# Kernel tuning notes

Hardware: AMD Instinct MI355X
Metric: run time of the kernel (lower is better)

## Reference

```python
import jax, jax.numpy as jnp
import numpy as np

B, S, D, DK = 4, 2048, 1024, 1024


def setup_inputs() -> dict:
    key = jax.random.key(0)
    kx, kq, kk, kv = jax.random.split(key, 4)
    return {
        "x": jax.random.normal(kx, (B, S, D), dtype=jnp.float32),
        "WQ": jax.random.normal(kq, (D, DK), dtype=jnp.float32),
        "WK": jax.random.normal(kk, (D, DK), dtype=jnp.float32),
        "WV": jax.random.normal(kv, (D, DK), dtype=jnp.float32),
    }


def reference(x, WQ, WK, WV):
    # q,k,v: [B,S,DK]
    q = x @ WQ
    k = x @ WK
    v = x @ WV
    scale = 1.0 / np.sqrt(DK).astype(np.float32)
    scores = jnp.einsum("bqd,bkd->bqk", q, k) * scale  # [B,S,S]
    # NOTE: original uses nn.Softmax(dim=1) -> normalize over the QUERY axis (axis 1)
    attn = jax.nn.softmax(scores, axis=1)
    return jnp.einsum("bqk,bkd->bqd", attn, v)
```

## Files before the change

kernel.cpp:

```cpp
#include <hip/hip_runtime.h>

constexpr int Bc  = 4;
constexpr int Sc  = 2048;
constexpr int Dc  = 1024;
constexpr int DKc = 1024;
constexpr long BSc = (long)Bc * Sc;

typedef __attribute__((ext_vector_type(8))) __bf16 bf16x8;
typedef __attribute__((ext_vector_type(4))) float  floatx4;

__device__ inline __bf16 f2bf(float f) {
  unsigned u = __builtin_bit_cast(unsigned, f);
  u = (u + 0x7FFFu + ((u >> 16) & 1u)) >> 16;
  unsigned short s = (unsigned short)u;
  return __builtin_bit_cast(__bf16, s);
}
__device__ inline float bf2f(__bf16 h) {
  unsigned u = ((unsigned)__builtin_bit_cast(unsigned short, h)) << 16;
  return __builtin_bit_cast(float, u);
}

__device__ inline void stage16(const __bf16* g, __bf16* l) {
  __builtin_amdgcn_global_load_lds(
      (const __attribute__((address_space(1))) unsigned int*)g,
      (__attribute__((address_space(3))) unsigned int*)l, 16, 0, 0);
}

__device__ __forceinline__ void bar_raw() {
  asm volatile("" ::: "memory");
  __builtin_amdgcn_s_barrier();
  asm volatile("" ::: "memory");
}
template <int N>
__device__ __forceinline__ void vmwait() {
  asm volatile("s_waitcnt vmcnt(%0)" :: "n"(N));
  __builtin_amdgcn_sched_barrier(0);
}

__global__ __launch_bounds__(256) void prep(
    const float* __restrict__ x,  __bf16* __restrict__ xhi, __bf16* __restrict__ xlo,
    const float* __restrict__ wq, __bf16* __restrict__ qhi, __bf16* __restrict__ qlo,
    const float* __restrict__ wk, __bf16* __restrict__ khi, __bf16* __restrict__ klo,
    const float* __restrict__ wv, __bf16* __restrict__ vthi) {
  __shared__ float tile[32][33];
  long blk = blockIdx.x;
  if (blk >= 40960) {
    int t   = (int)(blk - 40960);
    int bx  = t & 31, by = t >> 5;
    int thx = threadIdx.x & 31, thy = threadIdx.x >> 5;
    int xI  = bx * 32 + thx, yI = by * 32 + thy;
#pragma unroll
    for (int j = 0; j < 32; j += 8)
      tile[thy + j][thx] = wv[(long)(yI + j) * DKc + xI];
    __syncthreads();
    int xO = by * 32 + thx, yO = bx * 32 + thy;
#pragma unroll
    for (int j = 0; j < 32; j += 8)
      vthi[(long)(yO + j) * Dc + xO] = f2bf(tile[thx][thy + j]);
    return;
  }
  const float* in; __bf16 *hi, *lo; long base;
  if (blk < 32768)      { in = x;  hi = xhi; lo = xlo; base = blk * 256; }
  else if (blk < 36864) { in = wq; hi = qhi; lo = qlo; base = (blk - 32768) * 256; }
  else                  { in = wk; hi = khi; lo = klo; base = (blk - 36864) * 256; }
  long i = base + threadIdx.x;
  float f = in[i];
  __bf16 h = f2bf(f);
  hi[i] = h;
  lo[i] = f2bf(f - bf2f(h));
}

enum { MODE_V = 1 };
constexpr int VSTR = 136;

template <int MODE>
__device__ __forceinline__ void gemm_body(
    char* smem,
    const __bf16* __restrict__ Ahi,
    const __bf16* __restrict__ Bhi,
    __bf16* __restrict__ Chi) {
  constexpr int  K = Dc;
  __bf16* sAh = (__bf16*)smem;
  __bf16* sBh = sAh + 128 * 32;

  const int wave = threadIdx.x >> 6;
  const int lane = threadIdx.x & 63;
  const int wm   = wave >> 1;
  const int wn   = wave & 1;
  const int m0   = blockIdx.y * 128;
  const int n0   = blockIdx.x * 128;

  const __bf16* Ab  = Ahi + (long)m0 * K;
  const __bf16* Bb  = Bhi + (long)n0 * K;

  const int sr   = lane >> 2;
  const int sc_  = lane & 3;
  const int scol = (sc_ ^ ((sr >> 1) & 3)) * 8;

  floatx4 acc[4][4];
  const floatx4 zero = {0.f, 0.f, 0.f, 0.f};
#pragma unroll
  for (int i = 0; i < 4; ++i)
#pragma unroll
    for (int j = 0; j < 4; ++j) acc[i][j] = zero;

  const int frow = lane & 15;
  const int pko = ((lane >> 4) ^ ((frow >> 1) & 3)) * 8;

#pragma unroll 1
  for (int k0 = 0; k0 < K; k0 += 32) {
#pragma unroll
    for (int i = 0; i < 2; ++i) {
      const int rb = wave * 32 + i * 16;
      const long go = (long)(rb + sr) * K + k0 + scol;
      stage16(Ab + go, sAh + rb * 32);
      stage16(Bb + go, sBh + rb * 32);
    }
    __syncthreads();

    bf16x8 af[4], bfr[4];
#pragma unroll
    for (int t = 0; t < 4; ++t) {
      af[t]  = *(const bf16x8*)(sAh + (wm * 64 + t * 16 + frow) * 32 + pko);
      bfr[t] = *(const bf16x8*)(sBh + (wn * 64 + t * 16 + frow) * 32 + pko);
    }
#pragma unroll
    for (int mt = 0; mt < 4; ++mt)
#pragma unroll
      for (int nt = 0; nt < 4; ++nt)
        acc[mt][nt] = __builtin_amdgcn_mfma_f32_16x16x32_bf16(af[mt], bfr[nt], acc[mt][nt], 0, 0, 0);
    __syncthreads();
  }

  const int crow0 = (lane >> 4) * 4;
  const int ccol  = lane & 15;
  const int tid   = threadIdx.x;

  __bf16* sT = (__bf16*)smem;
#pragma unroll
  for (int nt = 0; nt < 4; ++nt) {
    int nl = wn * 64 + nt * 16 + ccol;
#pragma unroll
    for (int mt = 0; mt < 4; ++mt) {
      int ml = wm * 64 + mt * 16 + crow0;
#pragma unroll
      for (int r = 0; r < 4; ++r)
        sT[(long)nl * VSTR + ml + r] = f2bf(acc[mt][nt][r]);
    }
  }
  __syncthreads();
  const int bb   = m0 >> 11;
  const int seq0 = m0 & (Sc - 1);
  __bf16* dst = Chi + (long)bb * DKc * Sc + seq0;
#pragma unroll
  for (int c = 0; c < 8; ++c) {
    int flat = c * 2048 + tid * 8;
    int row = flat >> 7, col = flat & 127;
    *(bf16x8*)(dst + (long)(n0 + row) * Sc + col) =
        *(const bf16x8*)(sT + (long)row * VSTR + col);
  }
}

__global__ __launch_bounds__(256) void gemm_v(
    const __bf16* __restrict__ xhi, const __bf16* __restrict__ wvthi,
    __bf16* __restrict__ vt) {
  __shared__ __align__(16) char smem[128 * VSTR * 2];
  gemm_body<MODE_V>(smem, xhi, wvthi, vt);
}

struct SCtx {
  const __bf16 *pAh, *pAl, *pBh, *pBl;
  __bf16* lds;
  int stLds;
  int aoff, boff;
};

template <int WA, int WB, int WC, bool SAL, bool S2A, bool S2B>
__device__ __forceinline__ void tile_step(const SCtx& c, int t,
                                          floatx4 (&acc)[8][4]) {
  constexpr int K = 1024;
  constexpr int BH = 8192, BL = 16384, AL = 24576;
  __bf16* cur = c.lds + (t & 1) * 32768;
  __bf16* oth = c.lds + ((t & 1) ^ 1) * 32768;
  bf16x8 af[8], bfr[4];

  vmwait<WA>();
  bar_raw();
#pragma unroll
  for (int mt = 0; mt < 8; ++mt)
    af[mt] = *(const bf16x8*)(cur + c.aoff + mt * 512);
#pragma unroll
  for (int nt = 0; nt < 4; ++nt)
    bfr[nt] = *(const bf16x8*)(cur + BH + c.boff + nt * 512);
  if (SAL) {
    const __bf16* s = c.pAl + (t + 1) * 32;
    stage16(s, oth + AL + c.stLds);
    stage16(s + 16 * K, oth + AL + c.stLds + 512);
  }
  bar_raw();
  __builtin_amdgcn_s_setprio(1);
#pragma unroll
  for (int mt = 0; mt < 8; ++mt)
#pragma unroll
    for (int nt = 0; nt < 4; ++nt)
      acc[mt][nt] = __builtin_amdgcn_mfma_f32_16x16x32_bf16(af[mt], bfr[nt], acc[mt][nt], 0, 0, 0);
  __builtin_amdgcn_s_setprio(0);

  vmwait<WB>();
  bar_raw();
  {
    bf16x8 bfl[4];
#pragma unroll
    for (int nt = 0; nt < 4; ++nt)
      bfl[nt] = *(const bf16x8*)(cur + BL + c.boff + nt * 512);
    if (S2A) {
      const __bf16* sa = c.pAh + (t + 2) * 32;
      stage16(sa, cur + c.stLds);
      stage16(sa + 16 * K, cur + c.stLds + 512);
      stage16(c.pBh + (t + 2) * 32, cur + BH + c.stLds);
    }
    bar_raw();
    __builtin_amdgcn_s_setprio(1);
#pragma unroll
    for (int mt = 0; mt < 8; ++mt)
#pragma unroll
      for (int nt = 0; nt < 4; ++nt)
        acc[mt][nt] = __builtin_amdgcn_mfma_f32_16x16x32_bf16(af[mt], bfl[nt], acc[mt][nt], 0, 0, 0);
    __builtin_amdgcn_s_setprio(0);
  }

  vmwait<WC>();
  bar_raw();
  {
    bf16x8 afl[8];
#pragma unroll
    for (int mt = 0; mt < 8; ++mt)
      afl[mt] = *(const bf16x8*)(cur + AL + c.aoff + mt * 512);
    if (S2B) {
      stage16(c.pBh + (t + 2) * 32 + 16 * K, cur + BH + c.stLds + 512);
      const __bf16* sb = c.pBl + (t + 2) * 32;
      stage16(sb, cur + BL + c.stLds);
      stage16(sb + 16 * K, cur + BL + c.stLds + 512);
    }
    bar_raw();
    __builtin_amdgcn_s_setprio(1);
#pragma unroll
    for (int mt = 0; mt < 8; ++mt)
#pragma unroll
      for (int nt = 0; nt < 4; ++nt)
        acc[mt][nt] = __builtin_amdgcn_mfma_f32_16x16x32_bf16(afl[mt], bfr[nt], acc[mt][nt], 0, 0, 0);
    __builtin_amdgcn_s_setprio(0);
  }
}

__global__ __launch_bounds__(512, 2) void gemm_s2(
    const __bf16* __restrict__ thi, const __bf16* __restrict__ tlo,
    const __bf16* __restrict__ xhi, const __bf16* __restrict__ xlo,
    __bf16* __restrict__ P, float* __restrict__ Pmax, float* __restrict__ Psum) {
  __shared__ __align__(16) __bf16 smem[65536];
  constexpr int K = 1024;
  const int b    = blockIdx.z;
  const int m0   = blockIdx.y * 256;
  const int n0   = blockIdx.x * 256;
  const int wave = threadIdx.x >> 6;
  const int lane = threadIdx.x & 63;
  const int wm   = wave >> 2;
  const int wn   = wave & 3;
  const int sr   = lane >> 2;
  const int scol = ((lane & 3) ^ ((sr >> 1) & 3)) * 8;
  const int frow = lane & 15;
  const int pko  = ((lane >> 4) ^ ((frow >> 1) & 3)) * 8;

  SCtx c;
  const long batch = (long)Sc * 1024;
  const long ar = (long)(m0 + wave * 32 + sr) * K + scol;
  const long br = (long)(n0 + wave * 32 + sr) * K + scol;
  c.pAh = thi + (long)b * batch + ar;
  c.pAl = tlo + (long)b * batch + ar;
  c.pBh = xhi + (long)b * batch + br;
  c.pBl = xlo + (long)b * batch + br;
  c.lds = smem;
  c.stLds = wave * 1024;
  c.aoff = (wm * 128 + frow) * 32 + pko;
  c.boff = (wn * 64 + frow) * 32 + pko;

  {
    __bf16* b0 = smem;
    __bf16* b1 = smem + 32768;
    stage16(c.pAh, b0 + c.stLds);               stage16(c.pAh + 16 * K, b0 + c.stLds + 512);
    stage16(c.pBh, b0 + 8192 + c.stLds);        stage16(c.pBh + 16 * K, b0 + 8192 + c.stLds + 512);
    stage16(c.pBl, b0 + 16384 + c.stLds);       stage16(c.pBl + 16 * K, b0 + 16384 + c.stLds + 512);
    stage16(c.pAl, b0 + 24576 + c.stLds);       stage16(c.pAl + 16 * K, b0 + 24576 + c.stLds + 512);
    stage16(c.pAh + 32, b1 + c.stLds);          stage16(c.pAh + 32 + 16 * K, b1 + c.stLds + 512);
    stage16(c.pBh + 32, b1 + 8192 + c.stLds);   stage16(c.pBh + 32 + 16 * K, b1 + 8192 + c.stLds + 512);
    stage16(c.pBl + 32, b1 + 16384 + c.stLds);  stage16(c.pBl + 32 + 16 * K, b1 + 16384 + c.stLds + 512);
  }

  floatx4 acc[8][4];
  const floatx4 zero = {0.f, 0.f, 0.f, 0.f};
#pragma unroll
  for (int i = 0; i < 8; ++i)
#pragma unroll
    for (int j = 0; j < 4; ++j) acc[i][j] = zero;

#pragma unroll 1
  for (int t = 0; t < 30; ++t) tile_step<10, 10, 11, true, true, true>(c, t, acc);
  tile_step<10, 10, 8, true, false, false>(c, 30, acc);
  tile_step<4, 2, 0, false, false, false>(c, 31, acc);

  const int crow0 = (lane >> 4) * 4;
  const int ccol  = lane & 15;
  const int tid   = threadIdx.x;
  constexpr float scale = 0.03125f;
  float* smax = (float*)smem;
  float* ssum = smax + 512;

  float cm[4];
#pragma unroll
  for (int nt = 0; nt < 4; ++nt) {
    float mx = -3.0e38f;
#pragma unroll
    for (int mt = 0; mt < 8; ++mt)
#pragma unroll
      for (int r = 0; r < 4; ++r) mx = fmaxf(mx, acc[mt][nt][r] * scale);
    cm[nt] = mx;
  }
#pragma unroll
  for (int off = 16; off <= 32; off <<= 1)
#pragma unroll
    for (int nt = 0; nt < 4; ++nt)
      cm[nt] = fmaxf(cm[nt], __shfl_xor(cm[nt], off, 64));
  __syncthreads();
  if (lane < 16)
#pragma unroll
    for (int nt = 0; nt < 4; ++nt)
      smax[wm * 256 + wn * 64 + nt * 16 + lane] = cm[nt];
  __syncthreads();
  float mfin[4];
#pragma unroll
  for (int nt = 0; nt < 4; ++nt) {
    int cidx = wn * 64 + nt * 16 + ccol;
    mfin[nt] = fmaxf(smax[cidx], smax[256 + cidx]);
  }
  float ps[4];
#pragma unroll
  for (int nt = 0; nt < 4; ++nt) {
    float s = 0.f;
#pragma unroll
    for (int mt = 0; mt < 8; ++mt)
#pragma unroll
      for (int r = 0; r < 4; ++r)
        s += __expf(acc[mt][nt][r] * scale - mfin[nt]);
    ps[nt] = s;
  }
#pragma unroll
  for (int off = 16; off <= 32; off <<= 1)
#pragma unroll
    for (int nt = 0; nt < 4; ++nt) ps[nt] += __shfl_xor(ps[nt], off, 64);
  if (lane < 16)
#pragma unroll
    for (int nt = 0; nt < 4; ++nt)
      ssum[wm * 256 + wn * 64 + nt * 16 + lane] = ps[nt];
  __syncthreads();
  if (tid < 256) {
    long o = ((long)b * 8 + blockIdx.y) * Sc + n0 + tid;
    Pmax[o] = fmaxf(smax[tid], smax[256 + tid]);
    Psum[o] = ssum[tid] + ssum[256 + tid];
  }
  __syncthreads();
  __bf16* sT = smem;
#pragma unroll
  for (int nt = 0; nt < 4; ++nt) {
    int col = wn * 64 + nt * 16 + ccol;
#pragma unroll
    for (int mt = 0; mt < 8; ++mt) {
      int rowb = wm * 128 + mt * 16 + crow0;
#pragma unroll
      for (int r = 0; r < 4; ++r) {
        int row = rowb + r;
        sT[row * 256 + (col ^ (((row >> 2) & 3) << 4))] =
            f2bf(__expf(acc[mt][nt][r] * scale - mfin[nt]));
      }
    }
  }
  __syncthreads();
  __bf16* Pb = P + (long)b * ((long)Sc * Sc);
#pragma unroll
  for (int cc = 0; cc < 16; ++cc) {
    int flat = cc * 4096 + tid * 8;
    int row = flat >> 8, col = flat & 255;
    *(bf16x8*)(Pb + (long)(m0 + row) * Sc + n0 + col) =
        *(const bf16x8*)(sT + row * 256 + (col ^ (((row >> 2) & 3) << 4)));
  }
}

struct TCtx {
  const __bf16 *pAh, *pAl, *pBh, *pBl;
  __bf16* lds;
  int stA, stB;
  int aoff, boff;
};

template <int WA, int WB, int WC, bool SAL, bool S2AB, bool S2B>
__device__ __forceinline__ void tile_step_t(const TCtx& c, int t,
                                            floatx4 (&acc)[4][4]) {
  constexpr int K = 1024;
  constexpr int BH = 8192, BL = 12288, AL = 16384, BUF = 24576;
  __bf16* cur = c.lds + (t & 1) * BUF;
  __bf16* oth = c.lds + ((t & 1) ^ 1) * BUF;
  bf16x8 af[4], bfr[4];

  vmwait<WA>();
  bar_raw();
#pragma unroll
  for (int mt = 0; mt < 4; ++mt)
    af[mt] = *(const bf16x8*)(cur + c.aoff + mt * 512);
#pragma unroll
  for (int nt = 0; nt < 4; ++nt)
    bfr[nt] = *(const bf16x8*)(cur + BH + c.boff + nt * 512);
  if (SAL) {
    const __bf16* s = c.pAl + (t + 1) * 32;
    stage16(s, oth + AL + c.stA);
    stage16(s + 16 * K, oth + AL + c.stA + 512);
  }
  bar_raw();
  __builtin_amdgcn_s_setprio(1);
#pragma unroll
  for (int mt = 0; mt < 4; ++mt)
#pragma unroll
    for (int nt = 0; nt < 4; ++nt)
      acc[mt][nt] = __builtin_amdgcn_mfma_f32_16x16x32_bf16(af[mt], bfr[nt], acc[mt][nt], 0, 0, 0);
  __builtin_amdgcn_s_setprio(0);

  vmwait<WB>();
  bar_raw();
  {
    bf16x8 bfl[4];
#pragma unroll
    for (int nt = 0; nt < 4; ++nt)
      bfl[nt] = *(const bf16x8*)(cur + BL + c.boff + nt * 512);
    if (S2AB) {
      const __bf16* sa = c.pAh + (t + 2) * 32;
      stage16(sa, cur + c.stA);
      stage16(sa + 16 * K, cur + c.stA + 512);
      stage16(c.pBh + (t + 2) * 32, cur + BH + c.stB);
    }
    bar_raw();
    __builtin_amdgcn_s_setprio(1);
#pragma unroll
    for (int mt = 0; mt < 4; ++mt)
#pragma unroll
      for (int nt = 0; nt < 4; ++nt)
        acc[mt][nt] = __builtin_amdgcn_mfma_f32_16x16x32_bf16(af[mt], bfl[nt], acc[mt][nt], 0, 0, 0);
    __builtin_amdgcn_s_setprio(0);
  }

  vmwait<WC>();
  bar_raw();
  {
    bf16x8 afl[4];
#pragma unroll
    for (int mt = 0; mt < 4; ++mt)
      afl[mt] = *(const bf16x8*)(cur + AL + c.aoff + mt * 512);
    if (S2B) stage16(c.pBl + (t + 2) * 32, cur + BL + c.stB);
    bar_raw();
    __builtin_amdgcn_s_setprio(1);
#pragma unroll
    for (int mt = 0; mt < 4; ++mt)
#pragma unroll
      for (int nt = 0; nt < 4; ++nt)
        acc[mt][nt] = __builtin_amdgcn_mfma_f32_16x16x32_bf16(afl[mt], bfr[nt], acc[mt][nt], 0, 0, 0);
    __builtin_amdgcn_s_setprio(0);
  }
}

__global__ __launch_bounds__(512, 2) void gemm_t2(
    const __bf16* __restrict__ xhi, const __bf16* __restrict__ xlo,
    const __bf16* __restrict__ gthi, const __bf16* __restrict__ gtlo,
    __bf16* __restrict__ thi, __bf16* __restrict__ tlo) {
  __shared__ __align__(16) __bf16 smem[49152];
  constexpr int K = 1024;
  const int m0   = blockIdx.y * 256;
  const int n0   = blockIdx.x * 128;
  const int wave = threadIdx.x >> 6;
  const int lane = threadIdx.x & 63;
  const int wm   = wave >> 1;
  const int wn   = wave & 1;
  const int sr   = lane >> 2;
  const int scol = ((lane & 3) ^ ((sr >> 1) & 3)) * 8;
  const int frow = lane & 15;
  const int pko  = ((lane >> 4) ^ ((frow >> 1) & 3)) * 8;

  TCtx c;
  const long ar = (long)(m0 + wave * 32 + sr) * K + scol;
  const long br = (long)(n0 + wave * 16 + sr) * K + scol;
  c.pAh = xhi + ar;
  c.pAl = xlo + ar;
  c.pBh = gthi + br;
  c.pBl = gtlo + br;
  c.lds = smem;
  c.stA = wave * 1024;
  c.stB = wave * 512;
  c.aoff = (wm * 64 + frow) * 32 + pko;
  c.boff = (wn * 64 + frow) * 32 + pko;

  {
    __bf16* b0 = smem;
    __bf16* b1 = smem + 24576;
    stage16(c.pAh, b0 + c.stA);          stage16(c.pAh + 16 * K, b0 + c.stA + 512);
    stage16(c.pBh, b0 + 8192 + c.stB);
    stage16(c.pBl, b0 + 12288 + c.stB);
    stage16(c.pAl, b0 + 16384 + c.stA);  stage16(c.pAl + 16 * K, b0 + 16384 + c.stA + 512);
    stage16(c.pAh + 32, b1 + c.stA);     stage16(c.pAh + 32 + 16 * K, b1 + c.stA + 512);
    stage16(c.pBh + 32, b1 + 8192 + c.stB);
    stage16(c.pBl + 32, b1 + 12288 + c.stB);
  }

  floatx4 acc[4][4];
  const floatx4 zero = {0.f, 0.f, 0.f, 0.f};
#pragma unroll
  for (int i = 0; i < 4; ++i)
#pragma unroll
    for (int j = 0; j < 4; ++j) acc[i][j] = zero;

#pragma unroll 1
  for (int t = 0; t < 30; ++t) tile_step_t<7, 8, 9, true, true, true>(c, t, acc);
  tile_step_t<7, 8, 6, true, false, false>(c, 30, acc);
  tile_step_t<3, 2, 0, false, false, false>(c, 31, acc);

  const int crow0 = (lane >> 4) * 4;
  const int ccol  = lane & 15;
  const int tid   = threadIdx.x;
  __bf16* sT = smem;
#pragma unroll 1
  for (int pass = 0; pass < 2; ++pass) {
    __syncthreads();
#pragma unroll
    for (int nt = 0; nt < 4; ++nt) {
      int col = wn * 64 + nt * 16 + ccol;
#pragma unroll
      for (int mt = 0; mt < 4; ++mt) {
        int rowb = wm * 64 + mt * 16 + crow0;
#pragma unroll
        for (int r = 0; r < 4; ++r) {
          int row = rowb + r;
          float v = acc[mt][nt][r];
          __bf16 h = f2bf(v);
          sT[row * 128 + (col ^ (((row >> 2) & 3) << 4))] =
              pass ? f2bf(v - bf2f(h)) : h;
        }
      }
    }
    __syncthreads();
    __bf16* dst = pass ? tlo : thi;
#pragma unroll
    for (int cc = 0; cc < 8; ++cc) {
      int flat = cc * 4096 + tid * 8;
      int row = flat >> 7, col = flat & 127;
      *(bf16x8*)(dst + (long)(m0 + row) * DKc + n0 + col) =
          *(const bf16x8*)(sT + row * 128 + (col ^ (((row >> 2) & 3) << 4)));
    }
  }
}

__global__ __launch_bounds__(256) void scale_p(__bf16* __restrict__ P,
                                               const float* __restrict__ ffac) {
  long i8 = (long)blockIdx.x * 256 + threadIdx.x;
  long base = i8 * 8;
  int k = (int)(base & (Sc - 1));
  int q = (int)((base >> 11) & (Sc - 1));
  int b = (int)(base >> 22);
  int t = q >> 8;
  const float* f = ffac + (((long)b * 8 + t) << 11) + k;
  float4 f0 = *(const float4*)f;
  float4 f1 = *(const float4*)(f + 4);
  bf16x8 p = *(const bf16x8*)(P + base);
  bf16x8 o;
  o[0] = f2bf(bf2f(p[0]) * f0.x);
  o[1] = f2bf(bf2f(p[1]) * f0.y);
  o[2] = f2bf(bf2f(p[2]) * f0.z);
  o[3] = f2bf(bf2f(p[3]) * f0.w);
  o[4] = f2bf(bf2f(p[4]) * f1.x);
  o[5] = f2bf(bf2f(p[5]) * f1.y);
  o[6] = f2bf(bf2f(p[6]) * f1.z);
  o[7] = f2bf(bf2f(p[7]) * f1.w);
  *(bf16x8*)(P + base) = o;
}

struct PCtx {
  const __bf16 *pA, *pB;
  int stA, stB;
  int aoff, boff;
};

template <int WA, int WB, bool STG>
__device__ __forceinline__ void tile_step_pv(const PCtx& c, int t,
                                             __bf16* cur, __bf16* dst,
                                             floatx4 (&acc)[4][4]) {
  constexpr int K = 2048;
  vmwait<WA>();
  bar_raw();
  {
    bf16x8 af[4], bfr[4];
#pragma unroll
    for (int mt = 0; mt < 4; ++mt)
      af[mt] = *(const bf16x8*)(cur + c.aoff + mt * 512);
#pragma unroll
    for (int nt = 0; nt < 4; ++nt)
      bfr[nt] = *(const bf16x8*)(cur + 16384 + c.boff + nt * 512);
    if (STG) {
      const __bf16* a = c.pA + (t + 2) * 64;
      stage16(a, dst + c.stA);
      stage16(a + 16 * K, dst + c.stA + 512);
      stage16(c.pB + (t + 2) * 64, dst + 16384 + c.stB);
    }
    bar_raw();
    __builtin_amdgcn_s_setprio(1);
#pragma unroll
    for (int mt = 0; mt < 4; ++mt)
#pragma unroll
      for (int nt = 0; nt < 4; ++nt)
        acc[mt][nt] = __builtin_amdgcn_mfma_f32_16x16x32_bf16(af[mt], bfr[nt], acc[mt][nt], 0, 0, 0);
    __builtin_amdgcn_s_setprio(0);
  }
  vmwait<WB>();
  bar_raw();
  {
    bf16x8 af[4], bfr[4];
#pragma unroll
    for (int mt = 0; mt < 4; ++mt)
      af[mt] = *(const bf16x8*)(cur + 8192 + c.aoff + mt * 512);
#pragma unroll
    for (int nt = 0; nt < 4; ++nt)
      bfr[nt] = *(const bf16x8*)(cur + 20480 + c.boff + nt * 512);
    if (STG) {
      const __bf16* a = c.pA + (t + 2) * 64 + 32;
      stage16(a, dst + 8192 + c.stA);
      stage16(a + 16 * K, dst + 8192 + c.stA + 512);
      stage16(c.pB + (t + 2) * 64 + 32, dst + 20480 + c.stB);
    }
    bar_raw();
    __builtin_amdgcn_s_setprio(1);
#pragma unroll
    for (int mt = 0; mt < 4; ++mt)
#pragma unroll
      for (int nt = 0; nt < 4; ++nt)
        acc[mt][nt] = __builtin_amdgcn_mfma_f32_16x16x32_bf16(af[mt], bfr[nt], acc[mt][nt], 0, 0, 0);
    __builtin_amdgcn_s_setprio(0);
  }
}

__global__ __launch_bounds__(512, 2) void gemm_pv2(
    const __bf16* __restrict__ P, const __bf16* __restrict__ vt,
    float* __restrict__ out) {
  __shared__ __align__(16) __bf16 smem[73728];
  constexpr int K = 2048;
  const int b    = blockIdx.z;
  const int m0   = blockIdx.x * 256;
  const int n0   = blockIdx.y * 128;
  const int wave = threadIdx.x >> 6;
  const int lane = threadIdx.x & 63;
  const int wm   = wave >> 1;
  const int wn   = wave & 1;
  const int sr   = lane >> 2;
  const int scol = ((lane & 3) ^ ((sr >> 1) & 3)) * 8;
  const int frow = lane & 15;
  const int pko  = ((lane >> 4) ^ ((frow >> 1) & 3)) * 8;

  PCtx c;
  c.pA = P + (long)b * Sc * Sc + (long)(m0 + wave * 32 + sr) * K + scol;
  c.pB = vt + (long)b * DKc * Sc + (long)(n0 + wave * 16 + sr) * K + scol;
  c.stA = wave * 1024;
  c.stB = wave * 512;
  c.aoff = (wm * 64 + frow) * 32 + pko;
  c.boff = (wn * 64 + frow) * 32 + pko;

  __bf16* B0 = smem;
  __bf16* B1 = smem + 24576;
  __bf16* B2 = smem + 49152;

  stage16(c.pA, B0 + c.stA);            stage16(c.pA + 16 * K, B0 + c.stA + 512);
  stage16(c.pB, B0 + 16384 + c.stB);
  stage16(c.pA + 32, B0 + 8192 + c.stA); stage16(c.pA + 32 + 16 * K, B0 + 8192 + c.stA + 512);
  stage16(c.pB + 32, B0 + 20480 + c.stB);
  stage16(c.pA + 64, B1 + c.stA);       stage16(c.pA + 64 + 16 * K, B1 + c.stA + 512);
  stage16(c.pB + 64, B1 + 16384 + c.stB);
  stage16(c.pA + 96, B1 + 8192 + c.stA); stage16(c.pA + 96 + 16 * K, B1 + 8192 + c.stA + 512);
  stage16(c.pB + 96, B1 + 20480 + c.stB);

  floatx4 acc[4][4];
  const floatx4 zero = {0.f, 0.f, 0.f, 0.f};
#pragma unroll
  for (int i = 0; i < 4; ++i)
#pragma unroll
    for (int j = 0; j < 4; ++j) acc[i][j] = zero;

#pragma unroll 1
  for (int t = 0; t < 30; t += 3) {
    tile_step_pv<9, 9, true>(c, t,     B0, B2, acc);
    tile_step_pv<9, 9, true>(c, t + 1, B1, B0, acc);
    tile_step_pv<9, 9, true>(c, t + 2, B2, B1, acc);
  }
  tile_step_pv<9, 6, false>(c, 30, B0, B0, acc);
  tile_step_pv<3, 0, false>(c, 31, B1, B1, acc);

  const int crow0 = (lane >> 4) * 4;
  const int ccol  = lane & 15;
#pragma unroll
  for (int nt = 0; nt < 4; ++nt) {
    int cn = n0 + wn * 64 + nt * 16 + ccol;
#pragma unroll
    for (int mt = 0; mt < 4; ++mt) {
#pragma unroll
      for (int r = 0; r < 4; ++r) {
        int cm_ = m0 + wm * 64 + mt * 16 + crow0 + r;
        out[(long)b * Sc * DKc + (long)cm_ * DKc + cn] = acc[mt][nt][r];
      }
    }
  }
}

__global__ __launch_bounds__(256) void gemm_g64(
    const __bf16* __restrict__ Ahi, const __bf16* __restrict__ Alo,
    const __bf16* __restrict__ Bhi, const __bf16* __restrict__ Blo,
    __bf16* __restrict__ Chi, __bf16* __restrict__ Clo) {
  constexpr int K = Dc, N = DKc;
  __shared__ __align__(16) char smem[16384];
  __bf16* sAh = (__bf16*)smem;
  __bf16* sBh = sAh + 64 * 32;
  __bf16* sAl = sBh + 64 * 32;
  __bf16* sBl = sAl + 64 * 32;

  const int wave = threadIdx.x >> 6;
  const int lane = threadIdx.x & 63;
  const int wm   = wave >> 1, wn = wave & 1;
  const int m0   = blockIdx.y * 64;
  const int n0   = blockIdx.x * 64;

  const int sr   = lane >> 2;
  const int sc_  = lane & 3;
  const int scol = (sc_ ^ ((sr >> 1) & 3)) * 8;
  const int frow = lane & 15;
  const int pko  = ((lane >> 4) ^ ((frow >> 1) & 3)) * 8;

  floatx4 acc[2][2];
  const floatx4 zero = {0.f, 0.f, 0.f, 0.f};
#pragma unroll
  for (int i = 0; i < 2; ++i)
#pragma unroll
    for (int j = 0; j < 2; ++j) acc[i][j] = zero;

#pragma unroll 1
  for (int k0 = 0; k0 < K; k0 += 32) {
    const int rb = wave * 16;
    const long ga = (long)(m0 + rb + sr) * K + k0 + scol;
    const long gb = (long)(n0 + rb + sr) * K + k0 + scol;
    stage16(Ahi + ga, sAh + rb * 32);
    stage16(Alo + ga, sAl + rb * 32);
    stage16(Bhi + gb, sBh + rb * 32);
    stage16(Blo + gb, sBl + rb * 32);
    __syncthreads();

    bf16x8 af[2], bfr[2], afl[2], bfl[2];
#pragma unroll
    for (int t = 0; t < 2; ++t) {
      af[t]  = *(const bf16x8*)(sAh + (wm * 32 + t * 16 + frow) * 32 + pko);
      bfr[t] = *(const bf16x8*)(sBh + (wn * 32 + t * 16 + frow) * 32 + pko);
      afl[t] = *(const bf16x8*)(sAl + (wm * 32 + t * 16 + frow) * 32 + pko);
      bfl[t] = *(const bf16x8*)(sBl + (wn * 32 + t * 16 + frow) * 32 + pko);
    }
#pragma unroll
    for (int mt = 0; mt < 2; ++mt)
#pragma unroll
      for (int nt = 0; nt < 2; ++nt) {
        acc[mt][nt] = __builtin_amdgcn_mfma_f32_16x16x32_bf16(af[mt], bfr[nt], acc[mt][nt], 0, 0, 0);
        acc[mt][nt] = __builtin_amdgcn_mfma_f32_16x16x32_bf16(af[mt], bfl[nt], acc[mt][nt], 0, 0, 0);
        acc[mt][nt] = __builtin_amdgcn_mfma_f32_16x16x32_bf16(afl[mt], bfr[nt], acc[mt][nt], 0, 0, 0);
      }
    __syncthreads();
  }

  const int crow0 = (lane >> 4) * 4;
  const int ccol  = lane & 15;
  const int tid   = threadIdx.x;
  __bf16* sT = (__bf16*)smem;
#pragma unroll 1
  for (int pass = 0; pass < 2; ++pass) {
    __syncthreads();
#pragma unroll
    for (int nt = 0; nt < 2; ++nt) {
      int col = wn * 32 + nt * 16 + ccol;
#pragma unroll
      for (int mt = 0; mt < 2; ++mt) {
        int row = wm * 32 + mt * 16 + crow0;
#pragma unroll
        for (int r = 0; r < 4; ++r) {
          float v = acc[mt][nt][r];
          __bf16 h = f2bf(v);
          sT[(row + r) * 64 + col] = pass ? f2bf(v - bf2f(h)) : h;
        }
      }
    }
    __syncthreads();
    __bf16* dst = pass ? Clo : Chi;
#pragma unroll
    for (int c = 0; c < 2; ++c) {
      int flat = c * 2048 + tid * 8;
      int row = flat >> 6, col = flat & 63;
      *(bf16x8*)(dst + (long)(m0 + row) * N + n0 + col) = *(const bf16x8*)(sT + flat);
    }
  }
}

__global__ __launch_bounds__(256) void softmax_reduce(const float* __restrict__ Pmax,
                                                      const float* __restrict__ Psum,
                                                      float* __restrict__ Ffac) {
  int idx = blockIdx.x * 256 + threadIdx.x;
  int b = idx >> 11, k = idx & (Sc - 1);
  const float* pm = Pmax + (long)b * 8 * Sc + k;
  const float* ps = Psum + (long)b * 8 * Sc + k;
  float M = -3.0e38f;
#pragma unroll
  for (int t = 0; t < 8; ++t) M = fmaxf(M, pm[(long)t * Sc]);
  float S = 0.f;
#pragma unroll
  for (int t = 0; t < 8; ++t)
    S += ps[(long)t * Sc] * __expf(pm[(long)t * Sc] - M);
  float inv = 1.0f / S;
  float* fo = Ffac + (long)b * 8 * Sc + k;
#pragma unroll
  for (int t = 0; t < 8; ++t)
    fo[(long)t * Sc] = __expf(pm[(long)t * Sc] - M) * inv;
}

extern "C" void kernel_launch(void* const* d_in, const int* in_sizes, int n_in,
                              void* d_out, int out_size, void* d_ws, size_t ws_size,
                              hipStream_t stream) {
  const float* x  = (const float*)d_in[0];
  const float* WQ = (const float*)d_in[1];
  const float* WK = (const float*)d_in[2];
  const float* WV = (const float*)d_in[3];
  float* out = (float*)d_out;
  char* ws = (char*)d_ws;
  const long MB = 1024L * 1024L;

  __bf16* xhi  = (__bf16*)(ws + 0 * MB);
  __bf16* xlo  = (__bf16*)(ws + 16 * MB);
  __bf16* wqhi = (__bf16*)(ws + 32 * MB);
  __bf16* wqlo = (__bf16*)(ws + 34 * MB);
  __bf16* wkhi = (__bf16*)(ws + 36 * MB);
  __bf16* wklo = (__bf16*)(ws + 38 * MB);
  __bf16* wvthi= (__bf16*)(ws + 40 * MB);
  __bf16* gthi = (__bf16*)(ws + 44 * MB);
  __bf16* gtlo = (__bf16*)(ws + 46 * MB);
  __bf16* thi  = (__bf16*)(ws + 48 * MB);
  __bf16* tlo  = (__bf16*)(ws + 64 * MB);
  __bf16* vt   = (__bf16*)(ws + 80 * MB);
  __bf16* P    = (__bf16*)(ws + 96 * MB);
  float*  pmax = (float*)(ws + 128 * MB);
  float*  psum = (float*)(ws + 129 * MB);
  float*  ffac = (float*)(ws + 130 * MB);

  prep<<<41984, 256, 0, stream>>>(x, xhi, xlo, WQ, wqhi, wqlo, WK, wkhi, wklo,
                                  WV, wvthi);

  gemm_g64<<<dim3(16, 16), 256, 0, stream>>>(wkhi, wklo, wqhi, wqlo, gthi, gtlo);

  gemm_t2<<<dim3(DKc / 128, BSc / 256, 1), 512, 0, stream>>>(
      xhi, xlo, gthi, gtlo, thi, tlo);

  gemm_v<<<dim3(DKc / 128, BSc / 128, 1), 256, 0, stream>>>(xhi, wvthi, vt);

  gemm_s2<<<dim3(Sc / 256, Sc / 256, Bc), 512, 0, stream>>>(
      thi, tlo, xhi, xlo, P, pmax, psum);

  softmax_reduce<<<32, 256, 0, stream>>>(pmax, psum, ffac);

  scale_p<<<8192, 256, 0, stream>>>(P, ffac);

  gemm_pv2<<<dim3(Sc / 256, DKc / 128, Bc), 512, 0, stream>>>(P, vt, out);
}
```

Before: 341.5 us.

## Pipeline V projection GEMM with triple-buffered async staging and vectorize prep

Measured after the change: 327.2 us. -4.2%, faster.

```diff
diff --git a/kernel.cpp b/kernel.cpp
--- a/kernel.cpp
+++ b/kernel.cpp
@@ -7,6 +7,7 @@
 constexpr long BSc = (long)Bc * Sc;
 
 typedef __attribute__((ext_vector_type(8))) __bf16 bf16x8;
+typedef __attribute__((ext_vector_type(4))) __bf16 bf16x4;
 typedef __attribute__((ext_vector_type(4))) float  floatx4;
 
 __device__ inline __bf16 f2bf(float f) {
@@ -44,8 +45,8 @@
     const float* __restrict__ wv, __bf16* __restrict__ vthi) {
   __shared__ float tile[32][33];
   long blk = blockIdx.x;
-  if (blk >= 40960) {
-    int t   = (int)(blk - 40960);
+  if (blk >= 10240) {
+    int t   = (int)(blk - 10240);
     int bx  = t & 31, by = t >> 5;
     int thx = threadIdx.x & 31, thy = threadIdx.x >> 5;
     int xI  = bx * 32 + thx, yI = by * 32 + thy;
@@ -60,112 +61,17 @@
     return;
   }
   const float* in; __bf16 *hi, *lo; long base;
-  if (blk < 32768)      { in = x;  hi = xhi; lo = xlo; base = blk * 256; }
-  else if (blk < 36864) { in = wq; hi = qhi; lo = qlo; base = (blk - 32768) * 256; }
-  else                  { in = wk; hi = khi; lo = klo; base = (blk - 36864) * 256; }
-  long i = base + threadIdx.x;
-  float f = in[i];
-  __bf16 h = f2bf(f);
-  hi[i] = h;
-  lo[i] = f2bf(f - bf2f(h));
-}
-
-enum { MODE_V = 1 };
-constexpr int VSTR = 136;
-
-template <int MODE>
-__device__ __forceinline__ void gemm_body(
-    char* smem,
-    const __bf16* __restrict__ Ahi,
-    const __bf16* __restrict__ Bhi,
-    __bf16* __restrict__ Chi) {
-  constexpr int  K = Dc;
-  __bf16* sAh = (__bf16*)smem;
-  __bf16* sBh = sAh + 128 * 32;
-
-  const int wave = threadIdx.x >> 6;
-  const int lane = threadIdx.x & 63;
-  const int wm   = wave >> 1;
-  const int wn   = wave & 1;
-  const int m0   = blockIdx.y * 128;
-  const int n0   = blockIdx.x * 128;
-
-  const __bf16* Ab  = Ahi + (long)m0 * K;
-  const __bf16* Bb  = Bhi + (long)n0 * K;
-
-  const int sr   = lane >> 2;
-  const int sc_  = lane & 3;
-  const int scol = (sc_ ^ ((sr >> 1) & 3)) * 8;
-
-  floatx4 acc[4][4];
-  const floatx4 zero = {0.f, 0.f, 0.f, 0.f};
-#pragma unroll
-  for (int i = 0; i < 4; ++i)
-#pragma unroll
-    for (int j = 0; j < 4; ++j) acc[i][j] = zero;
-
-  const int frow = lane & 15;
-  const int pko = ((lane >> 4) ^ ((frow >> 1) & 3)) * 8;
-
-#pragma unroll 1
-  for (int k0 = 0; k0 < K; k0 += 32) {
-#pragma unroll
-    for (int i = 0; i < 2; ++i) {
-      const int rb = wave * 32 + i * 16;
-      const long go = (long)(rb + sr) * K + k0 + scol;
-      stage16(Ab + go, sAh + rb * 32);
-      stage16(Bb + go, sBh + rb * 32);
-    }
-    __syncthreads();
-
-    bf16x8 af[4], bfr[4];
-#pragma unroll
-    for (int t = 0; t < 4; ++t) {
-      af[t]  = *(const bf16x8*)(sAh + (wm * 64 + t * 16 + frow) * 32 + pko);
-      bfr[t] = *(const bf16x8*)(sBh + (wn * 64 + t * 16 + frow) * 32 + pko);
-    }
-#pragma unroll
-    for (int mt = 0; mt < 4; ++mt)
-#pragma unroll
-      for (int nt = 0; nt < 4; ++nt)
-        acc[mt][nt] = __builtin_amdgcn_mfma_f32_16x16x32_bf16(af[mt], bfr[nt], acc[mt][nt], 0, 0, 0);
-    __syncthreads();
-  }
-
-  const int crow0 = (lane >> 4) * 4;
-  const int ccol  = lane & 15;
-  const int tid   = threadIdx.x;
-
-  __bf16* sT = (__bf16*)smem;
-#pragma unroll
-  for (int nt = 0; nt < 4; ++nt) {
-    int nl = wn * 64 + nt * 16 + ccol;
-#pragma unroll
-    for (int mt = 0; mt < 4; ++mt) {
-      int ml = wm * 64 + mt * 16 + crow0;
-#pragma unroll
-      for (int r = 0; r < 4; ++r)
-        sT[(long)nl * VSTR + ml + r] = f2bf(acc[mt][nt][r]);
-    }
-  }
-  __syncthreads();
-  const int bb   = m0 >> 11;
-  const int seq0 = m0 & (Sc - 1);
-  __bf16* dst = Chi + (long)bb * DKc * Sc + seq0;
-#pragma unroll
-  for (int c = 0; c < 8; ++c) {
-    int flat = c * 2048 + tid * 8;
-    int row = flat >> 7, col = flat & 127;
-    *(bf16x8*)(dst + (long)(n0 + row) * Sc + col) =
-        *(const bf16x8*)(sT + (long)row * VSTR + col);
-  }
-}
-
-__global__ __launch_bounds__(256) void gemm_v(
-    const __bf16* __restrict__ xhi, const __bf16* __restrict__ wvthi,
-    __bf16* __restrict__ vt) {
-  __shared__ __align__(16) char smem[128 * VSTR * 2];
-  gemm_body<MODE_V>(smem, xhi, wvthi, vt);
+  if (blk < 8192)      { in = x;  hi = xhi; lo = xlo; base = blk * 1024; }
+  else if (blk < 9216) { in = wq; hi = qhi; lo = qlo; base = (blk - 8192) * 1024; }
+  else                 { in = wk; hi = khi; lo = klo; base = (blk - 9216) * 1024; }
+  long i = base + (long)threadIdx.x * 4;
+  float4 f = *(const float4*)(in + i);
+  __bf16 h0 = f2bf(f.x), h1 = f2bf(f.y), h2 = f2bf(f.z), h3 = f2bf(f.w);
+  bf16x4 hv = {h0, h1, h2, h3};
+  bf16x4 lv = {f2bf(f.x - bf2f(h0)), f2bf(f.y - bf2f(h1)),
+               f2bf(f.z - bf2f(h2)), f2bf(f.w - bf2f(h3))};
+  *(bf16x4*)(hi + i) = hv;
+  *(bf16x4*)(lo + i) = lv;
 }
 
 struct SCtx {
@@ -560,6 +466,68 @@
       *(bf16x8*)(dst + (long)(m0 + row) * DKc + n0 + col) =
           *(const bf16x8*)(sT + row * 128 + (col ^ (((row >> 2) & 3) << 4)));
     }
+  }
+}
+
+struct PCtx {
+  const __bf16 *pA, *pB;
+  int stA, stB;
+  int aoff, boff;
+};
+
+template <int KK, int WA, int WB, bool STG>
+__device__ __forceinline__ void tile_step_pv(const PCtx& c, int t,
+                                             __bf16* cur, __bf16* dst,
+                                             floatx4 (&acc)[4][4]) {
+  vmwait<WA>();
+  bar_raw();
+  {
+    bf16x8 af[4], bfr[4];
+#pragma unroll
+    for (int mt = 0; mt < 4; ++mt)
+      af[mt] = *(const bf16x8*)(cur + c.aoff + mt * 512);
+#pragma unroll
+    for (int nt = 0; nt < 4; ++nt)
+      bfr[nt] = *(const bf16x8*)(cur + 16384 + c.boff + nt * 512);
+    if (STG) {
+      const __bf16* a = c.pA + (t + 2) * 64;
+      stage16(a, dst + c.stA);
+      stage16(a + 16 * KK, dst + c.stA + 512);
+      stage16(c.pB + (t + 2) * 64, dst + 16384 + c.stB);
+    }
+    bar_raw();
+    __builtin_amdgcn_s_setprio(1);
+#pragma unroll
+    for (int mt = 0; mt < 4; ++mt)
+#pragma unroll
+      for (int nt = 0; nt < 4; ++nt)
+        acc[mt][nt] = __builtin_amdgcn_mfma_f32_16x16x32_bf16(af[mt], bfr[nt], acc[mt][nt], 0, 0, 0);
+    __builtin_amdgcn_s_setprio(0);
+  }
+  vmwait<WB>();
+  bar_raw();
+  {
+    bf16x8 af[4], bfr[4];
+#pragma unroll
+    for (int mt = 0; mt < 4; ++mt)
+      af[mt] = *(const bf16x8*)(cur + 8192 + c.aoff + mt * 512);
+#pragma unroll
+    for (int nt = 0; nt < 4; ++nt)
+      bfr[nt] = *(const bf16x8*)(cur + 20480 + c.boff + nt * 512);
+    if (STG) {
+      const __bf16* a = c.pA + (t + 2) * 64 + 32;
+      stage16(a, dst + 8192 + c.stA);
+      stage16(a + 16 * KK, dst + 8192 + c.stA + 512);
+      stage16(c.pB + (t + 2) * 64 + 32, dst + 20480 + c.stB);
+    }
+    bar_raw();
+    __builtin_amdgcn_s_setprio(1);
+#pragma unroll
+    for (int mt = 0; mt < 4; ++mt)
+#pragma unroll
+      for (int nt = 0; nt < 4; ++nt)
+        acc[mt][nt] = __builtin_amdgcn_mfma_f32_16x16x32_bf16(af[mt], bfr[nt], acc[mt][nt], 0, 0, 0);
+    __builtin_amdgcn_s_setprio(0);
   }
 }
 
@@ -587,69 +555,6 @@
   *(bf16x8*)(P + base) = o;
 }
 
-struct PCtx {
-  const __bf16 *pA, *pB;
-  int stA, stB;
-  int aoff, boff;
-};
-
-template <int WA, int WB, bool STG>
-__device__ __forceinline__ void tile_step_pv(const PCtx& c, int t,
-                                             __bf16* cur, __bf16* dst,
-                                             floatx4 (&acc)[4][4]) {
-  constexpr int K = 2048;
-  vmwait<WA>();
-  bar_raw();
-  {
-    bf16x8 af[4], bfr[4];
-#pragma unroll
-    for (int mt = 0; mt < 4; ++mt)
-      af[mt] = *(const bf16x8*)(cur + c.aoff + mt * 512);
-#pragma unroll
-    for (int nt = 0; nt < 4; ++nt)
-      bfr[nt] = *(const bf16x8*)(cur + 16384 + c.boff + nt * 512);
-    if (STG) {
-      const __bf16* a = c.pA + (t + 2) * 64;
-      stage16(a, dst + c.stA);
-      stage16(a + 16 * K, dst + c.stA + 512);
-      stage16(c.pB + (t + 2) * 64, dst + 16384 + c.stB);
-    }
-    bar_raw();
-    __builtin_amdgcn_s_setprio(1);
-#pragma unroll
-    for (int mt = 0; mt < 4; ++mt)
-#pragma unroll
-      for (int nt = 0; nt < 4; ++nt)
-        acc[mt][nt] = __builtin_amdgcn_mfma_f32_16x16x32_bf16(af[mt], bfr[nt], acc[mt][nt], 0, 0, 0);
-    __builtin_amdgcn_s_setprio(0);
-  }
-  vmwait<WB>();
-  bar_raw();
-  {
-    bf16x8 af[4], bfr[4];
-#pragma unroll
-    for (int mt = 0; mt < 4; ++mt)
-      af[mt] = *(const bf16x8*)(cur + 8192 + c.aoff + mt * 512);
-#pragma unroll
-    for (int nt = 0; nt < 4; ++nt)
-      bfr[nt] = *(const bf16x8*)(cur + 20480 + c.boff + nt * 512);
-    if (STG) {
-      const __bf16* a = c.pA + (t + 2) * 64 + 32;
-      stage16(a, dst + 8192 + c.stA);
-      stage16(a + 16 * K, dst + 8192 + c.stA + 512);
-      stage16(c.pB + (t + 2) * 64 + 32, dst + 20480 + c.stB);
-    }
-    bar_raw();
-    __builtin_amdgcn_s_setprio(1);
-#pragma unroll
-    for (int mt = 0; mt < 4; ++mt)
-#pragma unroll
-      for (int nt = 0; nt < 4; ++nt)
-        acc[mt][nt] = __builtin_amdgcn_mfma_f32_16x16x32_bf16(af[mt], bfr[nt], acc[mt][nt], 0, 0, 0);
-    __builtin_amdgcn_s_setprio(0);
-  }
-}
-
 __global__ __launch_bounds__(512, 2) void gemm_pv2(
     const __bf16* __restrict__ P, const __bf16* __restrict__ vt,
     float* __restrict__ out) {
@@ -697,12 +602,12 @@
 
 #pragma unroll 1
   for (int t = 0; t < 30; t += 3) {
-    tile_step_pv<9, 9, true>(c, t,     B0, B2, acc);
-    tile_step_pv<9, 9, true>(c, t + 1, B1, B0, acc);
-    tile_step_pv<9, 9, true>(c, t + 2, B2, B1, acc);
-  }
-  tile_step_pv<9, 6, false>(c, 30, B0, B0, acc);
-  tile_step_pv<3, 0, false>(c, 31, B1, B1, acc);
+    tile_step_pv<2048, 9, 9, true>(c, t,     B0, B2, acc);
+    tile_step_pv<2048, 9, 9, true>(c, t + 1, B1, B0, acc);
+    tile_step_pv<2048, 9, 9, true>(c, t + 2, B2, B1, acc);
+  }
+  tile_step_pv<2048, 9, 6, false>(c, 30, B0, B0, acc);
+  tile_step_pv<2048, 3, 0, false>(c, 31, B1, B1, acc);
 
   const int crow0 = (lane >> 4) * 4;
   const int ccol  = lane & 15;
@@ -717,6 +622,92 @@
         out[(long)b * Sc * DKc + (long)cm_ * DKc + cn] = acc[mt][nt][r];
       }
     }
+  }
+}
+
+constexpr int VSTR2 = 264;
+
+__global__ __launch_bounds__(512, 2) void gemm_v2(
+    const __bf16* __restrict__ xhi, const __bf16* __restrict__ wvthi,
+    __bf16* __restrict__ vt) {
+  __shared__ __align__(16) __bf16 smem[73728];
+  constexpr int K = 1024;
+  const int m0   = blockIdx.y * 256;
+  const int n0   = blockIdx.x * 128;
+  const int wave = threadIdx.x >> 6;
+  const int lane = threadIdx.x & 63;
+  const int wm   = wave >> 1;
+  const int wn   = wave & 1;
+  const int sr   = lane >> 2;
+  const int scol = ((lane & 3) ^ ((sr >> 1) & 3)) * 8;
+  const int frow = lane & 15;
+  const int pko  = ((lane >> 4) ^ ((frow >> 1) & 3)) * 8;
+
+  PCtx c;
+  c.pA = xhi + (long)(m0 + wave * 32 + sr) * K + scol;
+  c.pB = wvthi + (long)(n0 + wave * 16 + sr) * K + scol;
+  c.stA = wave * 1024;
+  c.stB = wave * 512;
+  c.aoff = (wm * 64 + frow) * 32 + pko;
+  c.boff = (wn * 64 + frow) * 32 + pko;
+
+  __bf16* B0 = smem;
+  __bf16* B1 = smem + 24576;
+  __bf16* B2 = smem + 49152;
+
+  stage16(c.pA, B0 + c.stA);            stage16(c.pA + 16 * K, B0 + c.stA + 512);
+  stage16(c.pB, B0 + 16384 + c.stB);
+  stage16(c.pA + 32, B0 + 8192 + c.stA); stage16(c.pA + 32 + 16 * K, B0 + 8192 + c.stA + 512);
+  stage16(c.pB + 32, B0 + 20480 + c.stB);
+  stage16(c.pA + 64, B1 + c.stA);       stage16(c.pA + 64 + 16 * K, B1 + c.stA + 512);
+  stage16(c.pB + 64, B1 + 16384 + c.stB);
+  stage16(c.pA + 96, B1 + 8192 + c.stA); stage16(c.pA + 96 + 16 * K, B1 + 8192 + c.stA + 512);
+  stage16(c.pB + 96, B1 + 20480 + c.stB);
+
+  floatx4 acc[4][4];
+  const floatx4 zero = {0.f, 0.f, 0.f, 0.f};
+#pragma unroll
+  for (int i = 0; i < 4; ++i)
+#pragma unroll
+    for (int j = 0; j < 4; ++j) acc[i][j] = zero;
+
+#pragma unroll 1
+  for (int t = 0; t < 12; t += 3) {
+    tile_step_pv<1024, 9, 9, true>(c, t,     B0, B2, acc);
+    tile_step_pv<1024, 9, 9, true>(c, t + 1, B1, B0, acc);
+    tile_step_pv<1024, 9, 9, true>(c, t + 2, B2, B1, acc);
+  }
+  tile_step_pv<1024, 9, 9, true >(c, 12, B0, B2, acc);
+  tile_step_pv<1024, 9, 9, true >(c, 13, B1, B0, acc);
+  tile_step_pv<1024, 9, 6, false>(c, 14, B2, B2, acc);
+  tile_step_pv<1024, 3, 0, false>(c, 15, B0, B0, acc);
+
+  const int crow0 = (lane >> 4) * 4;
+  const int ccol  = lane & 15;
+  const int tid   = threadIdx.x;
+  __syncthreads();
+  __bf16* sT = smem;
+#pragma unroll
+  for (int nt = 0; nt < 4; ++nt) {
+    int nl = wn * 64 + nt * 16 + ccol;
+#pragma unroll
+    for (int mt = 0; mt < 4; ++mt) {
+      int ml = wm * 64 + mt * 16 + crow0;
+#pragma unroll
+      for (int r = 0; r < 4; ++r)
+        sT[(long)nl * VSTR2 + ml + r] = f2bf(acc[mt][nt][r]);
+    }
+  }
+  __syncthreads();
+  const int bb   = m0 >> 11;
+  const int seq0 = m0 & (Sc - 1);
+  __bf16* dst = vt + (long)bb * DKc * Sc + seq0;
+#pragma unroll
+  for (int cc = 0; cc < 8; ++cc) {
+    int flat = cc * 4096 + tid * 8;
+    int row = flat >> 8, col = flat & 255;
+    *(bf16x8*)(dst + (long)(n0 + row) * Sc + col) =
+        *(const bf16x8*)(sT + (long)row * VSTR2 + col);
   }
 }
 
@@ -861,7 +852,7 @@
   float*  psum = (float*)(ws + 129 * MB);
   float*  ffac = (float*)(ws + 130 * MB);
 
-  prep<<<41984, 256, 0, stream>>>(x, xhi, xlo, WQ, wqhi, wqlo, WK, wkhi, wklo,
+  prep<<<11264, 256, 0, stream>>>(x, xhi, xlo, WQ, wqhi, wqlo, WK, wkhi, wklo,
                                   WV, wvthi);
 
   gemm_g64<<<dim3(16, 16), 256, 0, stream>>>(wkhi, wklo, wqhi, wqlo, gthi, gtlo);
@@ -869,7 +860,7 @@
   gemm_t2<<<dim3(DKc / 128, BSc / 256, 1), 512, 0, stream>>>(
       xhi, xlo, gthi, gtlo, thi, tlo);
 
-  gemm_v<<<dim3(DKc / 128, BSc / 128, 1), 256, 0, stream>>>(xhi, wvthi, vt);
+  gemm_v2<<<dim3(DKc / 128, BSc / 256, 1), 512, 0, stream>>>(xhi, wvthi, vt);
 
   gemm_s2<<<dim3(Sc / 256, Sc / 256, Bc), 512, 0, stream>>>(
       thi, tlo, xhi, xlo, P, pmax, psum);
```
